# Performance work log

Hardware: AMD Instinct MI355X
Metric: run time of the kernel (lower is better)

Reference implementation:

```python
import jax, jax.numpy as jnp
import numpy as np

N = 12288
IN_F = 256
OUT_F = 128
ALPHA = 0.2  # LeakyReLU negative slope


def setup_inputs() -> dict:
    key = jax.random.key(0)
    k_x, k_adj, k_w, k_a1, k_a2 = jax.random.split(key, 5)
    x = jax.random.normal(k_x, (N, IN_F), dtype=jnp.float32)
    adj = jax.random.randint(k_adj, (N, N), 0, 2, dtype=jnp.int32)
    # Learned params (nn.Linear without bias). Kaiming-uniform-ish init scale.
    W = jax.random.normal(k_w, (IN_F, OUT_F), dtype=jnp.float32) / np.sqrt(IN_F)
    a1 = jax.random.normal(k_a1, (OUT_F,), dtype=jnp.float32) / np.sqrt(OUT_F)
    a2 = jax.random.normal(k_a2, (OUT_F,), dtype=jnp.float32) / np.sqrt(OUT_F)
    return {"x": x, "adj": adj, "W": W, "a1": a1, "a2": a2}


def reference(x, adj, W, a1, a2):
    # h = tran(x): [N, OUT_F]
    h = x @ W
    # e[i, j] = att1(h)[j] + att2(h)[i]  (unsqueeze(0) + unsqueeze(1))
    s1 = h @ a1  # [N]
    s2 = h @ a2  # [N]
    e = s1[None, :] + s2[:, None]            # [N, N]
    e = jnp.where(e > 0, e, ALPHA * e)       # LeakyReLU
    e = jnp.where(adj > 0, e, -jnp.inf)      # mask non-edges
    attn = jax.nn.softmax(e, axis=1)         # row softmax (dropout=0 / eval)
    return attn @ h                          # [N, OUT_F]
```

## Files before the change

### kernel.cpp

```cpp
#include <hip/hip_runtime.h>
#include <hip/hip_bf16.h>

constexpr int NR = 12288;
constexpr int KF = 256;
constexpr int DF = 128;
constexpr int CH = 16;
constexpr int CW = NR / CH;
constexpr int NSTEP = CW / 32;
constexpr int ROWS = 128;
#define NEGBIG (-1e30f)

typedef __attribute__((ext_vector_type(8))) __bf16 bf16x8;
typedef __attribute__((ext_vector_type(4))) float  f32x4;

__device__ __forceinline__ unsigned short f2bf(float f) {
    union { float f; unsigned u; } v; v.f = f;
    unsigned r = v.u + 0x7FFFu + ((v.u >> 16) & 1u);
    return (unsigned short)(r >> 16);
}

__device__ __forceinline__ void gload16(const void* g, void* l) {
    __builtin_amdgcn_global_load_lds(
        (const __attribute__((address_space(1))) void*)g,
        (__attribute__((address_space(3))) void*)l, 16, 0, 0);
}

__global__ __launch_bounds__(256) void k_gemm_h(
    const float* __restrict__ x, const float* __restrict__ W,
    const float* __restrict__ a1, const float* __restrict__ a2,
    unsigned short* __restrict__ hbT, float* __restrict__ s1, float* __restrict__ s2)
{
    __shared__ __align__(16) float xs[64][65];
    __shared__ __align__(16) float ws[64][132];
    const int t  = threadIdx.x;
    const int tx = t & 15, ty = t >> 4;
    const int rowbase = blockIdx.x * 64;

    float acc[4][8];
#pragma unroll
    for (int i = 0; i < 4; ++i)
#pragma unroll
        for (int j = 0; j < 8; ++j) acc[i][j] = 0.f;

    for (int kt = 0; kt < KF; kt += 64) {
        {
            int row = t >> 2, k0 = (t & 3) * 16;
            const float4* src = (const float4*)(x + (size_t)(rowbase + row) * KF + kt + k0);
            float4 v0 = src[0], v1 = src[1], v2 = src[2], v3 = src[3];
            xs[row][k0+ 0]=v0.x; xs[row][k0+ 1]=v0.y; xs[row][k0+ 2]=v0.z; xs[row][k0+ 3]=v0.w;
            xs[row][k0+ 4]=v1.x; xs[row][k0+ 5]=v1.y; xs[row][k0+ 6]=v1.z; xs[row][k0+ 7]=v1.w;
            xs[row][k0+ 8]=v2.x; xs[row][k0+ 9]=v2.y; xs[row][k0+10]=v2.z; xs[row][k0+11]=v2.w;
            xs[row][k0+12]=v3.x; xs[row][k0+13]=v3.y; xs[row][k0+14]=v3.z; xs[row][k0+15]=v3.w;
        }
        {
            int k = t >> 2, c0 = (t & 3) * 32;
            const float4* src = (const float4*)(W + (size_t)(kt + k) * DF + c0);
#pragma unroll
            for (int j = 0; j < 8; ++j)
                *(float4*)&ws[k][c0 + j * 4] = src[j];
        }
        __syncthreads();
#pragma unroll 4
        for (int k = 0; k < 64; ++k) {
            float xv[4];
#pragma unroll
            for (int ri = 0; ri < 4; ++ri) xv[ri] = xs[ty * 4 + ri][k];
            float4 w0 = *(float4*)&ws[k][tx * 8];
            float4 w1 = *(float4*)&ws[k][tx * 8 + 4];
#pragma unroll
            for (int ri = 0; ri < 4; ++ri) {
                acc[ri][0] += xv[ri] * w0.x; acc[ri][1] += xv[ri] * w0.y;
                acc[ri][2] += xv[ri] * w0.z; acc[ri][3] += xv[ri] * w0.w;
                acc[ri][4] += xv[ri] * w1.x; acc[ri][5] += xv[ri] * w1.y;
                acc[ri][6] += xv[ri] * w1.z; acc[ri][7] += xv[ri] * w1.w;
            }
        }
        __syncthreads();
    }
#pragma unroll
    for (int ci = 0; ci < 8; ++ci) {
        int col = tx * 8 + ci;
        ushort4 u;
        u.x = f2bf(acc[0][ci]); u.y = f2bf(acc[1][ci]);
        u.z = f2bf(acc[2][ci]); u.w = f2bf(acc[3][ci]);
        *(ushort4*)(hbT + (size_t)col * NR + rowbase + ty * 4) = u;
    }
    float4 a1lo = *(const float4*)(a1 + tx * 8), a1hi = *(const float4*)(a1 + tx * 8 + 4);
    float4 a2lo = *(const float4*)(a2 + tx * 8), a2hi = *(const float4*)(a2 + tx * 8 + 4);
#pragma unroll
    for (int ri = 0; ri < 4; ++ri) {
        float p1 = acc[ri][0]*a1lo.x + acc[ri][1]*a1lo.y + acc[ri][2]*a1lo.z + acc[ri][3]*a1lo.w
                 + acc[ri][4]*a1hi.x + acc[ri][5]*a1hi.y + acc[ri][6]*a1hi.z + acc[ri][7]*a1hi.w;
        float p2 = acc[ri][0]*a2lo.x + acc[ri][1]*a2lo.y + acc[ri][2]*a2lo.z + acc[ri][3]*a2lo.w
                 + acc[ri][4]*a2hi.x + acc[ri][5]*a2hi.y + acc[ri][6]*a2hi.z + acc[ri][7]*a2hi.w;
#pragma unroll
        for (int off = 8; off > 0; off >>= 1) {
            p1 += __shfl_xor(p1, off);
            p2 += __shfl_xor(p2, off);
        }
        if (tx == 0) {
            s1[rowbase + ty * 4 + ri] = p1;
            s2[rowbase + ty * 4 + ri] = p2;
        }
    }
}

__global__ __launch_bounds__(1024) void k_gmax(
    const float* __restrict__ s1, float* __restrict__ gmax)
{
    __shared__ float red[16];
    const int t = threadIdx.x;
    float m = NEGBIG;
    const float4* s4 = (const float4*)s1;
    for (int i = t; i < NR / 4; i += 1024) {
        float4 v = s4[i];
        m = fmaxf(fmaxf(v.x, v.y), fmaxf(fmaxf(v.z, v.w), m));
    }
#pragma unroll
    for (int off = 32; off > 0; off >>= 1) m = fmaxf(m, __shfl_xor(m, off));
    if ((t & 63) == 0) red[t >> 6] = m;
    __syncthreads();
    if (t < 16) {
        m = red[t];
#pragma unroll
        for (int off = 8; off > 0; off >>= 1) m = fmaxf(m, __shfl_xor(m, off));
        if (t == 0) gmax[0] = m;
    }
}

__global__ __launch_bounds__(512, 4) void k_flash(
    const int* __restrict__ adj, const unsigned short* __restrict__ hbT,
    const float* __restrict__ s1, const float* __restrict__ s2,
    const float* __restrict__ gmaxp,
    float* __restrict__ num, float* __restrict__ lC)
{
    __shared__ __align__(16) int            adjring[3][4096];
    __shared__ __align__(16) unsigned short hbtring[3][4096];
    __shared__ __align__(16) float          s1lds[CW];

    const int t    = threadIdx.x;
    const int wid  = t >> 6, lane = t & 63;
    const int r    = lane & 15, g = lane >> 4;
    const int rowb = blockIdx.x * ROWS;
    const int prow = rowb + wid * 16 + r;
    const int chunk = blockIdx.y;
    const int j0 = chunk * CW;

    if (t < CW / 4) *(float4*)&s1lds[t * 4] = *(const float4*)(s1 + j0 + t * 4);

    const float gm  = gmaxp[0];
    const float s2r = s2[prow];
    const float zub = s2r + gm;
    const float Mi  = fmaxf(zub, 0.2f * zub);

    const int arow  = wid * 16 + (lane >> 3);
    const int acol4 = ((lane & 7) ^ (lane >> 3)) * 4;
    const int* agp0 = adj + (size_t)(rowb + arow) * NR + j0 + acol4;
    const int* agp1 = agp0 + (size_t)8 * NR;
    const int aldso0 = (wid * 16 + 0) * 128;
    const int aldso1 = (wid * 16 + 8) * 128;

    const int hrow  = wid * 16 + (lane >> 2);
    const int hcol8 = ((lane & 3) ^ ((lane >> 3) & 3)) * 8;
    const unsigned short* hgp0 = hbT + (size_t)hrow * NR + j0 + hcol8;
    const int hldso0 = wid * 16 * 64;

    const int a_off0 = (wid * 16 + r) * 128 + (((2 * g + 0) ^ (r & 7)) * 16);
    const int a_off1 = (wid * 16 + r) * 128 + (((2 * g + 1) ^ (r & 7)) * 16);
    const int h_base = r * 64 + ((g ^ ((r >> 1) & 3)) * 16);

#define ISSUE(st) do { \
        const int sl_ = (st) % 3; \
        const size_t go_ = (size_t)(((st) % NSTEP) * 32); \
        gload16(agp0 + go_, (char*)&adjring[sl_][0] + aldso0); \
        gload16(agp1 + go_, (char*)&adjring[sl_][0] + aldso1); \
        gload16(hgp0 + go_, (char*)&hbtring[sl_][0] + hldso0); \
    } while (0)

    float lsum = 0.f;
    f32x4 acc[8];
#pragma unroll
    for (int f = 0; f < 8; ++f) acc[f] = f32x4{0.f, 0.f, 0.f, 0.f};

    ISSUE(0);
    ISSUE(1);

    for (int j = 0; j < NSTEP; ++j) {
        asm volatile("s_waitcnt vmcnt(3) lgkmcnt(0)" ::: "memory");
        __builtin_amdgcn_s_barrier();
        __builtin_amdgcn_sched_barrier(0);
        ISSUE(j + 2);

        const int sl = j % 3;
        const int4 Aa = *(const int4*)((const char*)&adjring[sl][0] + a_off0);
        const int4 Ab = *(const int4*)((const char*)&adjring[sl][0] + a_off1);
        const float4 Sa = *(const float4*)&s1lds[j * 32 + g * 8];
        const float4 Sb = *(const float4*)&s1lds[j * 32 + g * 8 + 4];

        bf16x8 pf;
#define PROC(mm, ss, idx) { \
            float t0 = (ss) + s2r; \
            float lr = fmaxf(t0, 0.2f * t0); \
            float q  = __expf(lr - Mi); \
            float p  = ((mm) > 0) ? q : 0.f; \
            lsum += p; \
            pf[idx] = (__bf16)p; }
        PROC(Aa.x, Sa.x, 0) PROC(Aa.y, Sa.y, 1)
        PROC(Aa.z, Sa.z, 2) PROC(Aa.w, Sa.w, 3)
        PROC(Ab.x, Sb.x, 4) PROC(Ab.y, Sb.y, 5)
        PROC(Ab.z, Sb.z, 6) PROC(Ab.w, Sb.w, 7)
#undef PROC

        const char* hb = (const char*)&hbtring[sl][0] + h_base;
#pragma unroll
        for (int f = 0; f < 8; ++f) {
            bf16x8 bfr = *(const bf16x8*)(hb + f * 1024);
            acc[f] = __builtin_amdgcn_mfma_f32_16x16x32_bf16(pf, bfr, acc[f], 0, 0, 0);
        }
    }
#undef ISSUE

    lsum += __shfl_xor(lsum, 16);
    lsum += __shfl_xor(lsum, 32);
    if (g == 0) lC[(size_t)chunk * NR + prow] = lsum;

    float* nb = num + (size_t)chunk * NR * DF;
#pragma unroll
    for (int f = 0; f < 8; ++f)
#pragma unroll
        for (int q = 0; q < 4; ++q) {
            int row = rowb + wid * 16 + g * 4 + q;
            nb[(size_t)row * DF + f * 16 + r] = acc[f][q];
        }
}

__global__ __launch_bounds__(256) void k_comb(
    const float* __restrict__ num, const float* __restrict__ lC,
    float* __restrict__ out)
{
    const int t   = threadIdx.x;
    const int row = blockIdx.x * 2 + (t >> 7);
    const int f   = t & 127;
    float L = 0.f, o = 0.f;
    for (int c = 0; c < CH; ++c) {
        L += lC[(size_t)c * NR + row];
        o += num[(size_t)c * NR * DF + (size_t)row * DF + f];
    }
    out[(size_t)row * DF + f] = o / L;
}

extern "C" void kernel_launch(void* const* d_in, const int* in_sizes, int n_in,
                              void* d_out, int out_size, void* d_ws, size_t ws_size,
                              hipStream_t stream)
{
    const float* x   = (const float*)d_in[0];
    const int*   adj = (const int*)d_in[1];
    const float* W   = (const float*)d_in[2];
    const float* a1  = (const float*)d_in[3];
    const float* a2  = (const float*)d_in[4];
    float* out = (float*)d_out;

    char* p = (char*)d_ws;
    unsigned short* hbT = (unsigned short*)p; p += (size_t)DF * NR * 2;
    float*          s1  = (float*)p;          p += (size_t)NR * 4;
    float*          s2  = (float*)p;          p += (size_t)NR * 4;
    float*          gmx = (float*)p;          p += 256;
    float*          numb = (float*)p;         p += (size_t)CH * NR * DF * 4;
    float*          lC   = (float*)p;

    k_gemm_h<<<NR / 64, 256, 0, stream>>>(x, W, a1, a2, hbT, s1, s2);
    k_gmax<<<1, 1024, 0, stream>>>(s1, gmx);
    k_flash<<<dim3(NR / ROWS, CH), 512, 0, stream>>>(adj, hbT, s1, s2, gmx, numb, lC);
    k_comb<<<NR / 2, 256, 0, stream>>>(numb, lC, out);
}
```

Before: 227.6 us.

## Pre-pack adjacency into a bitmask and halve the column-chunk split

A new streaming kernel reads the int32 adjacency matrix once and packs it into a 1-bit-per-edge bitmask. The flash attention kernel then loads each block's bitmask rows into LDS once, instead of streaming int32 adjacency tiles through the global-to-LDS ring. This leaves only the h tiles in the pipeline, so the wait count drops. The chunk count falls from 16 to 8, which halves the partial numerator and denominator buffers that the combine kernel must write and read. The full adjacency is still read once, now in a separate kernel, and the change adds an extra launch and a bitmask round trip through memory.

```diff
diff --git a/kernel.cpp b/kernel.cpp
--- a/kernel.cpp
+++ b/kernel.cpp
@@ -4,10 +4,11 @@
 constexpr int NR = 12288;
 constexpr int KF = 256;
 constexpr int DF = 128;
-constexpr int CH = 16;
+constexpr int CH = 8;
 constexpr int CW = NR / CH;
 constexpr int NSTEP = CW / 32;
 constexpr int ROWS = 128;
+constexpr int BMW = NR / 32;
 #define NEGBIG (-1e30f)
 
 typedef __attribute__((ext_vector_type(8))) __bf16 bf16x8;
@@ -23,6 +24,27 @@
     __builtin_amdgcn_global_load_lds(
         (const __attribute__((address_space(1))) void*)g,
         (__attribute__((address_space(3))) void*)l, 16, 0, 0);
+}
+
+__global__ __launch_bounds__(256) void k_compress(
+    const int* __restrict__ adj, unsigned* __restrict__ bm)
+{
+    const int lane = threadIdx.x & 63;
+    const unsigned sh = (lane & 7) * 4;
+    size_t i = (size_t)blockIdx.x * 256 + threadIdx.x;
+    const size_t total4 = (size_t)NR * NR / 4;
+    const size_t stride = (size_t)gridDim.x * 256;
+    const int4* a4 = (const int4*)adj;
+    for (; i < total4; i += stride) {
+        int4 a = a4[i];
+        unsigned nib = (unsigned)(a.x > 0) | ((unsigned)(a.y > 0) << 1)
+                     | ((unsigned)(a.z > 0) << 2) | ((unsigned)(a.w > 0) << 3);
+        unsigned v = nib << sh;
+        v |= __shfl_xor(v, 1);
+        v |= __shfl_xor(v, 2);
+        v |= __shfl_xor(v, 4);
+        if ((lane & 7) == 0) bm[i >> 3] = v;
+    }
 }
 
 __global__ __launch_bounds__(256) void k_gemm_h(
@@ -129,13 +151,13 @@
 }
 
 __global__ __launch_bounds__(512, 4) void k_flash(
-    const int* __restrict__ adj, const unsigned short* __restrict__ hbT,
+    const unsigned* __restrict__ bm, const unsigned short* __restrict__ hbT,
     const float* __restrict__ s1, const float* __restrict__ s2,
     const float* __restrict__ gmaxp,
     float* __restrict__ num, float* __restrict__ lC)
 {
-    __shared__ __align__(16) int            adjring[3][4096];
     __shared__ __align__(16) unsigned short hbtring[3][4096];
+    __shared__ __align__(16) unsigned       bmlds[ROWS][52];
     __shared__ __align__(16) float          s1lds[CW];
 
     const int t    = threadIdx.x;
@@ -147,33 +169,28 @@
     const int j0 = chunk * CW;
 
     if (t < CW / 4) *(float4*)&s1lds[t * 4] = *(const float4*)(s1 + j0 + t * 4);
+#pragma unroll
+    for (int i = 0; i < 3; ++i) {
+        int idx = i * 512 + t;
+        int brow = idx / 12, bk = idx % 12;
+        uint4 w = *(const uint4*)(bm + (size_t)(rowb + brow) * BMW + chunk * NSTEP + bk * 4);
+        *(uint4*)&bmlds[brow][bk * 4] = w;
+    }
 
     const float gm  = gmaxp[0];
     const float s2r = s2[prow];
     const float zub = s2r + gm;
     const float Mi  = fmaxf(zub, 0.2f * zub);
 
-    const int arow  = wid * 16 + (lane >> 3);
-    const int acol4 = ((lane & 7) ^ (lane >> 3)) * 4;
-    const int* agp0 = adj + (size_t)(rowb + arow) * NR + j0 + acol4;
-    const int* agp1 = agp0 + (size_t)8 * NR;
-    const int aldso0 = (wid * 16 + 0) * 128;
-    const int aldso1 = (wid * 16 + 8) * 128;
-
     const int hrow  = wid * 16 + (lane >> 2);
     const int hcol8 = ((lane & 3) ^ ((lane >> 3) & 3)) * 8;
     const unsigned short* hgp0 = hbT + (size_t)hrow * NR + j0 + hcol8;
     const int hldso0 = wid * 16 * 64;
-
-    const int a_off0 = (wid * 16 + r) * 128 + (((2 * g + 0) ^ (r & 7)) * 16);
-    const int a_off1 = (wid * 16 + r) * 128 + (((2 * g + 1) ^ (r & 7)) * 16);
     const int h_base = r * 64 + ((g ^ ((r >> 1) & 3)) * 16);
 
 #define ISSUE(st) do { \
         const int sl_ = (st) % 3; \
         const size_t go_ = (size_t)(((st) % NSTEP) * 32); \
-        gload16(agp0 + go_, (char*)&adjring[sl_][0] + aldso0); \
-        gload16(agp1 + go_, (char*)&adjring[sl_][0] + aldso1); \
         gload16(hgp0 + go_, (char*)&hbtring[sl_][0] + hldso0); \
     } while (0)
 
@@ -185,32 +202,34 @@
     ISSUE(0);
     ISSUE(1);
 
+    const unsigned* bmrow = &bmlds[wid * 16 + r][0];
+    const unsigned gsh = g * 8;
+
     for (int j = 0; j < NSTEP; ++j) {
-        asm volatile("s_waitcnt vmcnt(3) lgkmcnt(0)" ::: "memory");
+        asm volatile("s_waitcnt vmcnt(1) lgkmcnt(0)" ::: "memory");
         __builtin_amdgcn_s_barrier();
         __builtin_amdgcn_sched_barrier(0);
         ISSUE(j + 2);
 
-        const int sl = j % 3;
-        const int4 Aa = *(const int4*)((const char*)&adjring[sl][0] + a_off0);
-        const int4 Ab = *(const int4*)((const char*)&adjring[sl][0] + a_off1);
+        const unsigned mw = bmrow[j] >> gsh;
         const float4 Sa = *(const float4*)&s1lds[j * 32 + g * 8];
         const float4 Sb = *(const float4*)&s1lds[j * 32 + g * 8 + 4];
 
         bf16x8 pf;
-#define PROC(mm, ss, idx) { \
+#define PROC(bi, ss, idx) { \
             float t0 = (ss) + s2r; \
             float lr = fmaxf(t0, 0.2f * t0); \
             float q  = __expf(lr - Mi); \
-            float p  = ((mm) > 0) ? q : 0.f; \
+            float p  = ((mw >> (bi)) & 1u) ? q : 0.f; \
             lsum += p; \
             pf[idx] = (__bf16)p; }
-        PROC(Aa.x, Sa.x, 0) PROC(Aa.y, Sa.y, 1)
-        PROC(Aa.z, Sa.z, 2) PROC(Aa.w, Sa.w, 3)
-        PROC(Ab.x, Sb.x, 4) PROC(Ab.y, Sb.y, 5)
-        PROC(Ab.z, Sb.z, 6) PROC(Ab.w, Sb.w, 7)
+        PROC(0, Sa.x, 0) PROC(1, Sa.y, 1)
+        PROC(2, Sa.z, 2) PROC(3, Sa.w, 3)
+        PROC(4, Sb.x, 4) PROC(5, Sb.y, 5)
+        PROC(6, Sb.z, 6) PROC(7, Sb.w, 7)
 #undef PROC
 
+        const int sl = j % 3;
         const char* hb = (const char*)&hbtring[sl][0] + h_base;
 #pragma unroll
         for (int f = 0; f < 8; ++f) {
@@ -262,14 +281,16 @@
 
     char* p = (char*)d_ws;
     unsigned short* hbT = (unsigned short*)p; p += (size_t)DF * NR * 2;
+    unsigned*       bmw = (unsigned*)p;       p += (size_t)NR * BMW * 4;
     float*          s1  = (float*)p;          p += (size_t)NR * 4;
     float*          s2  = (float*)p;          p += (size_t)NR * 4;
     float*          gmx = (float*)p;          p += 256;
     float*          numb = (float*)p;         p += (size_t)CH * NR * DF * 4;
     float*          lC   = (float*)p;
 
+    k_compress<<<2048, 256, 0, stream>>>(adj, bmw);
     k_gemm_h<<<NR / 64, 256, 0, stream>>>(x, W, a1, a2, hbT, s1, s2);
     k_gmax<<<1, 1024, 0, stream>>>(s1, gmx);
-    k_flash<<<dim3(NR / ROWS, CH), 512, 0, stream>>>(adj, hbT, s1, s2, gmx, numb, lC);
+    k_flash<<<dim3(NR / ROWS, CH), 512, 0, stream>>>(bmw, hbT, s1, s2, gmx, numb, lC);
     k_comb<<<NR / 2, 256, 0, stream>>>(numb, lC, out);
 }
```

Result: no change. 229.8 us (+1.0%).

## Keep h chunk resident in LDS across six row subtiles, store partials as fp16

Applied to the files above, without the earlier changes.

The flash kernel now loads its whole column chunk of transposed h (128 features by 384 columns, padded stride) into LDS once. It then loops over six 128-row subtiles, streaming only adj through the triple-buffered ring, so h is no longer re-fetched for every 128-row block. The column split doubles from 16 to 32 chunks to keep the grid large. Partial numerators are written as fp16 to halve combine traffic, at the cost of more chunk partials, larger LDS use (lower occupancy) and reduced precision.

```diff
diff --git a/kernel.cpp b/kernel.cpp
--- a/kernel.cpp
+++ b/kernel.cpp
@@ -1,13 +1,16 @@
 #include <hip/hip_runtime.h>
 #include <hip/hip_bf16.h>
+#include <hip/hip_fp16.h>
 
 constexpr int NR = 12288;
 constexpr int KF = 256;
 constexpr int DF = 128;
-constexpr int CH = 16;
+constexpr int CH = 32;
 constexpr int CW = NR / CH;
-constexpr int NSTEP = CW / 32;
-constexpr int ROWS = 128;
+constexpr int RG = 768;
+constexpr int NSS = RG / 128;
+constexpr int KSS = CW / 32;
+constexpr int HSTRIDE = 784;
 #define NEGBIG (-1e30f)
 
 typedef __attribute__((ext_vector_type(8))) __bf16 bf16x8;
@@ -128,114 +131,119 @@
     }
 }
 
-__global__ __launch_bounds__(512, 4) void k_flash(
+__global__ __launch_bounds__(512) void k_flash(
     const int* __restrict__ adj, const unsigned short* __restrict__ hbT,
     const float* __restrict__ s1, const float* __restrict__ s2,
     const float* __restrict__ gmaxp,
-    float* __restrict__ num, float* __restrict__ lC)
-{
-    __shared__ __align__(16) int            adjring[3][4096];
-    __shared__ __align__(16) unsigned short hbtring[3][4096];
-    __shared__ __align__(16) float          s1lds[CW];
+    __half* __restrict__ num, float* __restrict__ lC)
+{
+    __shared__ __align__(16) char  hbt[128 * HSTRIDE];
+    __shared__ __align__(16) int   adjring[3][128 * 32];
+    __shared__ __align__(16) float s1lds[CW];
 
     const int t    = threadIdx.x;
     const int wid  = t >> 6, lane = t & 63;
     const int r    = lane & 15, g = lane >> 4;
-    const int rowb = blockIdx.x * ROWS;
-    const int prow = rowb + wid * 16 + r;
+    const int rowb  = blockIdx.x * RG;
     const int chunk = blockIdx.y;
     const int j0 = chunk * CW;
 
     if (t < CW / 4) *(float4*)&s1lds[t * 4] = *(const float4*)(s1 + j0 + t * 4);
-
-    const float gm  = gmaxp[0];
-    const float s2r = s2[prow];
-    const float zub = s2r + gm;
-    const float Mi  = fmaxf(zub, 0.2f * zub);
+#pragma unroll
+    for (int i = 0; i < 12; ++i) {
+        int idx  = i * 512 + t;
+        int feat = idx / 48, c = idx % 48;
+        bf16x8 v = *(const bf16x8*)(hbT + (size_t)feat * NR + j0 + c * 8);
+        *(bf16x8*)&hbt[feat * HSTRIDE + c * 16] = v;
+    }
+
+    const float gm = gmaxp[0];
 
     const int arow  = wid * 16 + (lane >> 3);
     const int acol4 = ((lane & 7) ^ (lane >> 3)) * 4;
-    const int* agp0 = adj + (size_t)(rowb + arow) * NR + j0 + acol4;
-    const int* agp1 = agp0 + (size_t)8 * NR;
+    const int* agp  = adj + (size_t)(rowb + arow) * NR + j0 + acol4;
     const int aldso0 = (wid * 16 + 0) * 128;
     const int aldso1 = (wid * 16 + 8) * 128;
-
-    const int hrow  = wid * 16 + (lane >> 2);
-    const int hcol8 = ((lane & 3) ^ ((lane >> 3) & 3)) * 8;
-    const unsigned short* hgp0 = hbT + (size_t)hrow * NR + j0 + hcol8;
-    const int hldso0 = wid * 16 * 64;
-
     const int a_off0 = (wid * 16 + r) * 128 + (((2 * g + 0) ^ (r & 7)) * 16);
     const int a_off1 = (wid * 16 + r) * 128 + (((2 * g + 1) ^ (r & 7)) * 16);
-    const int h_base = r * 64 + ((g ^ ((r >> 1) & 3)) * 16);
-
-#define ISSUE(st) do { \
-        const int sl_ = (st) % 3; \
-        const size_t go_ = (size_t)(((st) % NSTEP) * 32); \
-        gload16(agp0 + go_, (char*)&adjring[sl_][0] + aldso0); \
-        gload16(agp1 + go_, (char*)&adjring[sl_][0] + aldso1); \
-        gload16(hgp0 + go_, (char*)&hbtring[sl_][0] + hldso0); \
+    const int h_lane = r * HSTRIDE + g * 16;
+
+#define ISSUE(s_, j_) do { \
+        const int sl_ = ((s_) * KSS + (j_)) % 3; \
+        const size_t go_ = (size_t)(s_) * 128 * NR + (size_t)(j_) * 32; \
+        gload16(agp + go_, (char*)&adjring[sl_][0] + aldso0); \
+        gload16(agp + go_ + (size_t)8 * NR, (char*)&adjring[sl_][0] + aldso1); \
     } while (0)
 
-    float lsum = 0.f;
-    f32x4 acc[8];
-#pragma unroll
-    for (int f = 0; f < 8; ++f) acc[f] = f32x4{0.f, 0.f, 0.f, 0.f};
-
-    ISSUE(0);
-    ISSUE(1);
-
-    for (int j = 0; j < NSTEP; ++j) {
-        asm volatile("s_waitcnt vmcnt(3) lgkmcnt(0)" ::: "memory");
-        __builtin_amdgcn_s_barrier();
-        __builtin_amdgcn_sched_barrier(0);
-        ISSUE(j + 2);
-
-        const int sl = j % 3;
-        const int4 Aa = *(const int4*)((const char*)&adjring[sl][0] + a_off0);
-        const int4 Ab = *(const int4*)((const char*)&adjring[sl][0] + a_off1);
-        const float4 Sa = *(const float4*)&s1lds[j * 32 + g * 8];
-        const float4 Sb = *(const float4*)&s1lds[j * 32 + g * 8 + 4];
-
-        bf16x8 pf;
+    ISSUE(0, 0);
+    ISSUE(0, 1);
+    int s2i = 0, j2i = 2;
+
+    for (int s = 0; s < NSS; ++s) {
+        const int srow = rowb + s * 128 + wid * 16 + r;
+        const float s2r = s2[srow];
+        const float zub = s2r + gm;
+        const float Mi  = fmaxf(zub, 0.2f * zub);
+
+        float lsum = 0.f;
+        f32x4 acc[8];
+#pragma unroll
+        for (int f = 0; f < 8; ++f) acc[f] = f32x4{0.f, 0.f, 0.f, 0.f};
+
+        for (int j = 0; j < KSS; ++j) {
+            const int it = s * KSS + j;
+            asm volatile("s_waitcnt vmcnt(2) lgkmcnt(0)" ::: "memory");
+            __builtin_amdgcn_s_barrier();
+            __builtin_amdgcn_sched_barrier(0);
+            if (j2i >= 0) { ISSUE(s2i, j2i); }
+            if (++j2i == KSS) { j2i = 0; if (++s2i == NSS) { s2i = 0; j2i = -1; } }
+
+            const int sl = it % 3;
+            const int4 Aa = *(const int4*)((const char*)&adjring[sl][0] + a_off0);
+            const int4 Ab = *(const int4*)((const char*)&adjring[sl][0] + a_off1);
+            const float4 Sa = *(const float4*)&s1lds[j * 32 + g * 8];
+            const float4 Sb = *(const float4*)&s1lds[j * 32 + g * 8 + 4];
+
+            bf16x8 pf;
 #define PROC(mm, ss, idx) { \
-            float t0 = (ss) + s2r; \
-            float lr = fmaxf(t0, 0.2f * t0); \
-            float q  = __expf(lr - Mi); \
-            float p  = ((mm) > 0) ? q : 0.f; \
-            lsum += p; \
-            pf[idx] = (__bf16)p; }
-        PROC(Aa.x, Sa.x, 0) PROC(Aa.y, Sa.y, 1)
-        PROC(Aa.z, Sa.z, 2) PROC(Aa.w, Sa.w, 3)
-        PROC(Ab.x, Sb.x, 4) PROC(Ab.y, Sb.y, 5)
-        PROC(Ab.z, Sb.z, 6) PROC(Ab.w, Sb.w, 7)
+                float t0 = (ss) + s2r; \
+                float lr = fmaxf(t0, 0.2f * t0); \
+                float q  = __expf(lr - Mi); \
+                float p  = ((mm) > 0) ? q : 0.f; \
+                lsum += p; \
+                pf[idx] = (__bf16)p; }
+            PROC(Aa.x, Sa.x, 0) PROC(Aa.y, Sa.y, 1)
+            PROC(Aa.z, Sa.z, 2) PROC(Aa.w, Sa.w, 3)
+            PROC(Ab.x, Sb.x, 4) PROC(Ab.y, Sb.y, 5)
+            PROC(Ab.z, Sb.z, 6) PROC(Ab.w, Sb.w, 7)
 #undef PROC
 
-        const char* hb = (const char*)&hbtring[sl][0] + h_base;
-#pragma unroll
-        for (int f = 0; f < 8; ++f) {
-            bf16x8 bfr = *(const bf16x8*)(hb + f * 1024);
-            acc[f] = __builtin_amdgcn_mfma_f32_16x16x32_bf16(pf, bfr, acc[f], 0, 0, 0);
-        }
+            const char* hb = hbt + h_lane + j * 64;
+#pragma unroll
+            for (int f = 0; f < 8; ++f) {
+                bf16x8 bfr = *(const bf16x8*)(hb + f * (16 * HSTRIDE));
+                acc[f] = __builtin_amdgcn_mfma_f32_16x16x32_bf16(pf, bfr, acc[f], 0, 0, 0);
+            }
+        }
+
+        lsum += __shfl_xor(lsum, 16);
+        lsum += __shfl_xor(lsum, 32);
+        if (g == 0) lC[(size_t)chunk * NR + srow] = lsum;
+
+        __half* nb = num + (size_t)chunk * NR * DF;
+#pragma unroll
+        for (int f = 0; f < 8; ++f)
+#pragma unroll
+            for (int q = 0; q < 4; ++q) {
+                int row = rowb + s * 128 + wid * 16 + g * 4 + q;
+                nb[(size_t)row * DF + f * 16 + r] = __float2half(acc[f][q]);
+            }
     }
 #undef ISSUE
-
-    lsum += __shfl_xor(lsum, 16);
-    lsum += __shfl_xor(lsum, 32);
-    if (g == 0) lC[(size_t)chunk * NR + prow] = lsum;
-
-    float* nb = num + (size_t)chunk * NR * DF;
-#pragma unroll
-    for (int f = 0; f < 8; ++f)
-#pragma unroll
-        for (int q = 0; q < 4; ++q) {
-            int row = rowb + wid * 16 + g * 4 + q;
-            nb[(size_t)row * DF + f * 16 + r] = acc[f][q];
-        }
 }
 
 __global__ __launch_bounds__(256) void k_comb(
-    const float* __restrict__ num, const float* __restrict__ lC,
+    const __half* __restrict__ num, const float* __restrict__ lC,
     float* __restrict__ out)
 {
     const int t   = threadIdx.x;
@@ -244,7 +252,7 @@
     float L = 0.f, o = 0.f;
     for (int c = 0; c < CH; ++c) {
         L += lC[(size_t)c * NR + row];
-        o += num[(size_t)c * NR * DF + (size_t)row * DF + f];
+        o += __half2float(num[(size_t)c * NR * DF + (size_t)row * DF + f]);
     }
     out[(size_t)row * DF + f] = o / L;
 }
@@ -265,11 +273,11 @@
     float*          s1  = (float*)p;          p += (size_t)NR * 4;
     float*          s2  = (float*)p;          p += (size_t)NR * 4;
     float*          gmx = (float*)p;          p += 256;
-    float*          numb = (float*)p;         p += (size_t)CH * NR * DF * 4;
+    __half*         numb = (__half*)p;        p += (size_t)CH * NR * DF * 2;
     float*          lC   = (float*)p;
 
     k_gemm_h<<<NR / 64, 256, 0, stream>>>(x, W, a1, a2, hbT, s1, s2);
     k_gmax<<<1, 1024, 0, stream>>>(s1, gmx);
-    k_flash<<<dim3(NR / ROWS, CH), 512, 0, stream>>>(adj, hbT, s1, s2, gmx, numb, lC);
+    k_flash<<<dim3(NR / RG, CH), 512, 0, stream>>>(adj, hbT, s1, s2, gmx, numb, lC);
     k_comb<<<NR / 2, 256, 0, stream>>>(numb, lC, out);
 }
```

Result: slower. 282.6 us (+24.2%).
